# Optimization experiments

Measured on AMD Instinct MI355X. Metric: run time of the kernel, lower is better.

## Reference

```python
import jax, jax.numpy as jnp
import numpy as np

B = 64          # batch of trees
L = 10          # gated internal levels below the root
H = 256         # hidden_size
E = 256         # embed_size
V = 64          # embedding vocab (relation/role types)
TOTAL = 2 ** (L + 1) - 2   # heap layout: level i (1..L) has 2^i nodes at offset 2^i - 2


def setup_inputs() -> dict:
    key = jax.random.key(0)
    k = jax.random.split(key, 7)
    s = 0.05
    return {
        "node_ids": jax.random.randint(k[0], (B, TOTAL), 0, V, dtype=jnp.int32),
        "emb_table": jax.random.normal(k[1], (V, E), jnp.float32) * s,
        # W: x-projections, order (forget, input, output, update)
        "W": jax.random.normal(k[2], (4, E, H), jnp.float32) * s,
        "bW": jax.random.normal(k[3], (4, H), jnp.float32) * s,
        # U: hidden projections, [gate, child] with gate order
        # (forget_left, forget_right, input, output, update), child order (left, right)
        "U": jax.random.normal(k[4], (5, 2, H, H), jnp.float32) * s,
        "Ws": jax.random.normal(k[5], (2 * H, 3), jnp.float32) * s,
        "bs": jax.random.normal(k[6], (3,), jnp.float32) * s,
    }


def _tree_lstm(node_ids, emb_table, W, bW, U, Ws, bs):
    Bn, total = node_ids.shape
    Lv = int(np.log2(total + 2)) - 1          # number of gated levels (static)
    Hh = U.shape[-1]
    # Wforget is shared by both forget gates (as in the original module)
    gate_map = jnp.array([0, 0, 1, 2, 3])      # x-projection index per gate
    h = c = None
    for lev in range(Lv, 0, -1):               # leaves-up level order
        n = 2 ** lev
        off = 2 ** lev - 2
        ids = node_ids[:, off:off + n]         # [B, n]
        x = emb_table[ids]                     # [B, n, E]
        xg = jnp.einsum('bne,geh->gbnh', x, W) + bW[:, None, None, :]  # [4,B,n,H]
        if h is None:
            # deepest level: children are leaves -> zero h and c (init_hidden())
            hl = hr = cl = cr = jnp.zeros((Bn, n, Hh), x.dtype)
        else:
            hl, hr = h[:, 0::2], h[:, 1::2]
            cl, cr = c[:, 0::2], c[:, 1::2]
        pre = (jnp.einsum('bnh,ghk->gbnk', hl, U[:, 0])
               + jnp.einsum('bnh,ghk->gbnk', hr, U[:, 1])
               + xg[gate_map])                 # [5,B,n,H]
        f_l = jax.nn.sigmoid(pre[0])
        f_r = jax.nn.sigmoid(pre[1])
        i_g = jax.nn.sigmoid(pre[2])
        o_g = jax.nn.sigmoid(pre[3])
        u_g = jnp.tanh(pre[4])
        c = i_g * u_g + f_l * cl + f_r * cr
        h = o_g * jnp.tanh(c)
    # root: concatenate the two children's hidden states, then score
    root_hidden = jnp.concatenate([h[:, 0], h[:, 1]], axis=-1)   # [B, 2H]
    scores = root_hidden @ Ws + bs                               # [B, 3]
    return scores, root_hidden


def reference(node_ids, emb_table, W, bW, U, Ws, bs):
    return _tree_lstm(node_ids, emb_table, W, bW, U, Ws, bs)
```

## Files before the change

### kernel.cpp

```cpp
#include <hip/hip_runtime.h>
#include <hip/hip_bf16.h>
#include <stdint.h>
#include <math.h>


typedef __bf16 bf16x8 __attribute__((ext_vector_type(8)));
typedef float  f32x4  __attribute__((ext_vector_type(4)));
typedef int    i32x4  __attribute__((ext_vector_type(4)));

__device__ __forceinline__ float sigf(float x) { return 1.f / (1.f + __expf(-x)); }
__device__ __forceinline__ float tanhfast(float x) {
    return 1.f - 2.f / (__expf(2.f * x) + 1.f);
}

__global__ void xg_prep(const float* __restrict__ emb, const float* __restrict__ W,
                        const float* __restrict__ bW, float* __restrict__ xg4) {
    int g = blockIdx.x >> 6, v = blockIdx.x & 63, k = threadIdx.x;
    __shared__ float e[256];
    e[k] = emb[v * 256 + k];
    __syncthreads();
    float s = bW[g * 256 + k];
    const float* Wg = W + g * 65536 + k;
#pragma unroll 4
    for (int i = 0; i < 256; i++) s += e[i] * Wg[i * 256];
    xg4[(v * 256 + k) * 4 + g] = s;
}

__global__ void bt_prep(const float* __restrict__ U, __bf16* __restrict__ BtP) {
    int t = blockIdx.x * 256 + threadIdx.x;
    int g    = t >> 14;
    int r    = t & 16383;
    int ct   = r >> 10;
    int ks   = (r >> 6) & 15;
    int lane = t & 63;
    int lr = lane & 15, q = lane >> 4;
    int col = ct * 16 + lr;
    int kbase = ks * 32 + q * 8;
    bf16x8 v8;
#pragma unroll
    for (int e = 0; e < 8; e++) {
        int k = kbase + e;
        int s = k >> 8, kk = k & 255;
        v8[e] = (__bf16)U[((g * 2 + s) * 256 + kk) * 256 + col];
    }
    *(bf16x8*)(BtP + (long)t * 8) = v8;
}

__global__ void leaf_kernel(const int* __restrict__ ids, const float* __restrict__ xg4,
                            __bf16* __restrict__ h, __bf16* __restrict__ c) {
    int col = threadIdx.x;
    int r0 = blockIdx.x * 32;
    for (int r = r0; r < r0 + 32; r++) {
        int b = r >> 10, j = r & 1023;
        int id = ids[b * 2046 + 1022 + j];
        f32x4 xv = *(const f32x4*)(xg4 + (id * 256 + col) * 4);
        float ig = sigf(xv.y);
        float og = sigf(xv.z);
        float ug = tanhfast(xv.w);
        float cv = ig * ug;
        float hv = og * tanhfast(cv);
        h[r * 256 + col] = (__bf16)hv;
        c[r * 256 + col] = (__bf16)cv;
    }
}

__global__ __launch_bounds__(1024, 4) void level_kernel(
    const __bf16* __restrict__ A, const __bf16* __restrict__ Cprev,
    const __bf16* __restrict__ BtP, const float* __restrict__ xg4,
    const int* __restrict__ ids, __bf16* __restrict__ h_out,
    __bf16* __restrict__ c_out, float* __restrict__ rh_out, int lev, int M, int RG) {
    __shared__ __bf16 Blds[5 * 16 * 512];
    const int gid = blockIdx.x;
    int rg, ct;
    if ((RG & 7) == 0) {
        int xcd = gid & 7;
        int t   = gid >> 3;
        ct = t & 15;
        rg = ((t >> 4) << 3) | xcd;
    } else {
        rg = gid >> 4;
        ct = gid & 15;
    }
    const int tid  = threadIdx.x;
    const int wave = tid >> 6;
    const int lane = tid & 63;
    const int lr = lane & 15, q = lane >> 4;
    const long wrow = (long)rg * 512 + wave * 32;
    const bool active = (wrow < M);

#pragma unroll
    for (int i = 0; i < 5; i++) {
        int c = tid + i * 1024;
        int g = c >> 10;
        int r = c & 1023;
        i32x4 v = *(const i32x4*)(BtP + (long)(g * 16 + ct) * 8192 + r * 8);
        *(i32x4*)(&Blds[g * 8192 + r * 8]) = v;
    }

    const __bf16* Ap = A + (wrow + lr) * 512 + q * 8;
    bf16x8 af[4][2];
    if (active) {
#pragma unroll
        for (int mt = 0; mt < 2; mt++) {
            af[0][mt] = *(const bf16x8*)(Ap + mt * 8192);
            af[1][mt] = *(const bf16x8*)(Ap + mt * 8192 + 32);
            af[2][mt] = *(const bf16x8*)(Ap + mt * 8192 + 64);
        }
    }

    const int n = 1 << lev;
    const int gcol = ct * 16 + lr;
    int idv[2][4];
    __bf16 clv[2][4], crv[2][4];
    if (active) {
#pragma unroll
        for (int mt = 0; mt < 2; mt++)
#pragma unroll
            for (int v = 0; v < 4; v++) {
                long grow = wrow + mt * 16 + q * 4 + v;
                int b = (int)(grow >> lev);
                int j = (int)(grow & (n - 1));
                idv[mt][v] = ids[b * 2046 + (n - 2) + j];
                clv[mt][v] = Cprev[grow * 512 + gcol];
                crv[mt][v] = Cprev[grow * 512 + 256 + gcol];
            }
    }

    __syncthreads();

    if (active) {
        f32x4 acc[5][2];
#pragma unroll
        for (int g2 = 0; g2 < 5; g2++)
#pragma unroll
            for (int mt = 0; mt < 2; mt++) acc[g2][mt] = (f32x4){0.f, 0.f, 0.f, 0.f};

        bf16x8 bb[2][5];
#pragma unroll
        for (int g2 = 0; g2 < 5; g2++)
            bb[0][g2] = *(const bf16x8*)(&Blds[g2 * 8192 + lane * 8]);

#pragma unroll
        for (int s = 0; s < 16; s++) {
            if (s + 3 < 16) {
#pragma unroll
                for (int mt = 0; mt < 2; mt++)
                    af[(s + 3) & 3][mt] =
                        *(const bf16x8*)(Ap + mt * 8192 + (s + 3) * 32);
            }
            if (s + 1 < 16) {
#pragma unroll
                for (int g2 = 0; g2 < 5; g2++)
                    bb[(s + 1) & 1][g2] =
                        *(const bf16x8*)(&Blds[g2 * 8192 + (s + 1) * 512 + lane * 8]);
            }
#pragma unroll
            for (int g2 = 0; g2 < 5; g2++)
#pragma unroll
                for (int mt = 0; mt < 2; mt++)
                    acc[g2][mt] = __builtin_amdgcn_mfma_f32_16x16x32_bf16(
                        af[s & 3][mt], bb[s & 1][g2], acc[g2][mt], 0, 0, 0);
        }

#pragma unroll
        for (int mt = 0; mt < 2; mt++) {
#pragma unroll
            for (int v = 0; v < 4; v++) {
                long grow = wrow + mt * 16 + q * 4 + v;
                f32x4 xv = *(const f32x4*)(xg4 + (idv[mt][v] * 256 + gcol) * 4);
                float fl = sigf(acc[0][mt][v] + xv.x);
                float fr = sigf(acc[1][mt][v] + xv.x);
                float ig = sigf(acc[2][mt][v] + xv.y);
                float og = sigf(acc[3][mt][v] + xv.z);
                float ug = tanhfast(acc[4][mt][v] + xv.w);
                float cv = ig * ug + fl * (float)clv[mt][v] + fr * (float)crv[mt][v];
                float hv = og * tanhfast(cv);
                h_out[grow * 256 + gcol] = (__bf16)hv;
                c_out[grow * 256 + gcol] = (__bf16)cv;
                if (rh_out) rh_out[grow * 256 + gcol] = hv;
            }
        }
    }
}

__global__ void scores_kernel(const float* __restrict__ rh, const float* __restrict__ Ws,
                              const float* __restrict__ bs, float* __restrict__ out) {
    int b = blockIdx.x;
    int t = threadIdx.x >> 6, lane = threadIdx.x & 63;
    float s = 0.f;
    for (int i = lane; i < 512; i += 64) s += rh[b * 512 + i] * Ws[i * 3 + t];
    for (int o = 32; o > 0; o >>= 1) s += __shfl_down(s, o);
    if (lane == 0) out[b * 3 + t] = s + bs[t];
}

extern "C" void kernel_launch(void* const* d_in, const int* in_sizes, int n_in,
                              void* d_out, int out_size, void* d_ws, size_t ws_size,
                              hipStream_t stream) {
    const int*   ids = (const int*)  d_in[0];
    const float* emb = (const float*)d_in[1];
    const float* W   = (const float*)d_in[2];
    const float* bW  = (const float*)d_in[3];
    const float* U   = (const float*)d_in[4];
    const float* Ws  = (const float*)d_in[5];
    const float* bs  = (const float*)d_in[6];
    float* out = (float*)d_out;

    char* ws = (char*)d_ws;
    float*  xg4 = (float*)ws;
    __bf16* BtP = (__bf16*)(ws + 262144);
    __bf16* h0  = (__bf16*)(ws + 1572864);
    __bf16* c0  = (__bf16*)(ws + 35127296);
    __bf16* h1  = (__bf16*)(ws + 68681728);
    __bf16* c1  = (__bf16*)(ws + 85458944);

    xg_prep<<<dim3(256), dim3(256), 0, stream>>>(emb, W, bW, xg4);
    bt_prep<<<dim3(320), dim3(256), 0, stream>>>(U, BtP);
    leaf_kernel<<<dim3(2048), dim3(256), 0, stream>>>(ids, xg4, h0, c0);

    __bf16* hb[2] = {h0, h1};
    __bf16* cb[2] = {c0, c1};
    int cur = 0;
    for (int lev = 9; lev >= 1; lev--) {
        int M = 64 << lev;
        int RG = (M + 511) / 512;
        float* rh = (lev == 1) ? (out + 192) : nullptr;
        level_kernel<<<dim3(RG * 16), dim3(1024), 0, stream>>>(
            hb[cur], cb[cur], BtP, xg4, ids, hb[1 - cur], cb[1 - cur], rh, lev, M, RG);
        cur = 1 - cur;
    }
    scores_kernel<<<dim3(64), dim3(192), 0, stream>>>(out + 192, Ws, bs, out);
}
```

Baseline: 430.8 us.

## Fuse per-level launches into one persistent cooperative kernel with grid sync

Replaces nine separate level_kernel launches with a single cooperative persistent kernel of 256 blocks. Each block loads its column tile of U into LDS once, then loops over levels and row groups, separating levels with a threadfence plus grid.sync. This removes repeated launch and LDS reload costs, at the price of grid-wide barriers and fewer blocks on the large early levels. The A and B fragment prefetch is also changed to a three-stage ring.

```diff
diff --git a/kernel.cpp b/kernel.cpp
--- a/kernel.cpp
+++ b/kernel.cpp
@@ -1,8 +1,11 @@
 #include <hip/hip_runtime.h>
+#include <hip/hip_cooperative_groups.h>
 #include <hip/hip_bf16.h>
 #include <stdint.h>
 #include <math.h>
 
+
+namespace cg = cooperative_groups;
 
 typedef __bf16 bf16x8 __attribute__((ext_vector_type(8)));
 typedef float  f32x4  __attribute__((ext_vector_type(4)));
@@ -64,122 +67,127 @@
     }
 }
 
-__global__ __launch_bounds__(1024, 4) void level_kernel(
-    const __bf16* __restrict__ A, const __bf16* __restrict__ Cprev,
+__global__ __launch_bounds__(1024, 4) void tree_levels(
+    __bf16* __restrict__ h0, __bf16* __restrict__ c0,
+    __bf16* __restrict__ h1, __bf16* __restrict__ c1,
     const __bf16* __restrict__ BtP, const float* __restrict__ xg4,
-    const int* __restrict__ ids, __bf16* __restrict__ h_out,
-    __bf16* __restrict__ c_out, float* __restrict__ rh_out, int lev, int M, int RG) {
+    const int* __restrict__ ids, float* __restrict__ rh_base) {
     __shared__ __bf16 Blds[5 * 16 * 512];
-    const int gid = blockIdx.x;
-    int rg, ct;
-    if ((RG & 7) == 0) {
-        int xcd = gid & 7;
-        int t   = gid >> 3;
-        ct = t & 15;
-        rg = ((t >> 4) << 3) | xcd;
-    } else {
-        rg = gid >> 4;
-        ct = gid & 15;
-    }
+    cg::grid_group grid = cg::this_grid();
+
+    const int pid  = blockIdx.x;
+    const int xcd  = pid & 7;
+    const int ct   = (pid >> 3) & 15;
+    const int slot = pid >> 7;
     const int tid  = threadIdx.x;
     const int wave = tid >> 6;
     const int lane = tid & 63;
     const int lr = lane & 15, q = lane >> 4;
-    const long wrow = (long)rg * 512 + wave * 32;
-    const bool active = (wrow < M);
+    const int gcol = ct * 16 + lr;
 
 #pragma unroll
     for (int i = 0; i < 5; i++) {
-        int c = tid + i * 1024;
-        int g = c >> 10;
-        int r = c & 1023;
-        i32x4 v = *(const i32x4*)(BtP + (long)(g * 16 + ct) * 8192 + r * 8);
-        *(i32x4*)(&Blds[g * 8192 + r * 8]) = v;
-    }
-
-    const __bf16* Ap = A + (wrow + lr) * 512 + q * 8;
-    bf16x8 af[4][2];
-    if (active) {
-#pragma unroll
-        for (int mt = 0; mt < 2; mt++) {
-            af[0][mt] = *(const bf16x8*)(Ap + mt * 8192);
-            af[1][mt] = *(const bf16x8*)(Ap + mt * 8192 + 32);
-            af[2][mt] = *(const bf16x8*)(Ap + mt * 8192 + 64);
-        }
-    }
-
-    const int n = 1 << lev;
-    const int gcol = ct * 16 + lr;
-    int idv[2][4];
-    __bf16 clv[2][4], crv[2][4];
-    if (active) {
-#pragma unroll
-        for (int mt = 0; mt < 2; mt++)
-#pragma unroll
-            for (int v = 0; v < 4; v++) {
-                long grow = wrow + mt * 16 + q * 4 + v;
-                int b = (int)(grow >> lev);
-                int j = (int)(grow & (n - 1));
-                idv[mt][v] = ids[b * 2046 + (n - 2) + j];
-                clv[mt][v] = Cprev[grow * 512 + gcol];
-                crv[mt][v] = Cprev[grow * 512 + 256 + gcol];
-            }
-    }
-
+        int cc = tid + i * 1024;
+        int g = cc >> 10;
+        int r = cc & 1023;
+        *(i32x4*)(&Blds[g * 8192 + r * 8]) =
+            *(const i32x4*)(BtP + (long)(g * 16 + ct) * 8192 + r * 8);
+    }
     __syncthreads();
 
-    if (active) {
-        f32x4 acc[5][2];
-#pragma unroll
-        for (int g2 = 0; g2 < 5; g2++)
-#pragma unroll
-            for (int mt = 0; mt < 2; mt++) acc[g2][mt] = (f32x4){0.f, 0.f, 0.f, 0.f};
-
-        bf16x8 bb[2][5];
-#pragma unroll
-        for (int g2 = 0; g2 < 5; g2++)
-            bb[0][g2] = *(const bf16x8*)(&Blds[g2 * 8192 + lane * 8]);
-
-#pragma unroll
-        for (int s = 0; s < 16; s++) {
-            if (s + 3 < 16) {
+    for (int lev = 9; lev >= 1; lev--) {
+        const int M  = 64 << lev;
+        const int RG = (M + 511) >> 9;
+        const int p  = (9 - lev) & 1;
+        const __bf16* A  = p ? h1 : h0;
+        const __bf16* Cp = p ? c1 : c0;
+        __bf16* Ho = p ? h0 : h1;
+        __bf16* Co = p ? c0 : c1;
+        float* rh = (lev == 1) ? rh_base : nullptr;
+        const int n = 1 << lev;
+
+        for (int rg = xcd + 8 * slot; rg < RG; rg += 16) {
+            const long wrow = (long)rg * 512 + wave * 32;
+            if (wrow < M) {
+                const __bf16* Ap = A + (wrow + lr) * 512 + q * 8;
+                bf16x8 af[3][2];
+#pragma unroll
+                for (int mt = 0; mt < 2; mt++) {
+                    af[0][mt] = *(const bf16x8*)(Ap + mt * 8192);
+                    af[1][mt] = *(const bf16x8*)(Ap + mt * 8192 + 32);
+                }
+
+                int idv[2][4];
+                __bf16 clv[2][4], crv[2][4];
 #pragma unroll
                 for (int mt = 0; mt < 2; mt++)
-                    af[(s + 3) & 3][mt] =
-                        *(const bf16x8*)(Ap + mt * 8192 + (s + 3) * 32);
-            }
-            if (s + 1 < 16) {
+#pragma unroll
+                    for (int v = 0; v < 4; v++) {
+                        long grow = wrow + mt * 16 + q * 4 + v;
+                        int b = (int)(grow >> lev);
+                        int j = (int)(grow & (n - 1));
+                        idv[mt][v] = ids[b * 2046 + (n - 2) + j];
+                        clv[mt][v] = Cp[grow * 512 + gcol];
+                        crv[mt][v] = Cp[grow * 512 + 256 + gcol];
+                    }
+
+                f32x4 acc[5][2];
 #pragma unroll
                 for (int g2 = 0; g2 < 5; g2++)
-                    bb[(s + 1) & 1][g2] =
-                        *(const bf16x8*)(&Blds[g2 * 8192 + (s + 1) * 512 + lane * 8]);
-            }
-#pragma unroll
-            for (int g2 = 0; g2 < 5; g2++)
-#pragma unroll
-                for (int mt = 0; mt < 2; mt++)
-                    acc[g2][mt] = __builtin_amdgcn_mfma_f32_16x16x32_bf16(
-                        af[s & 3][mt], bb[s & 1][g2], acc[g2][mt], 0, 0, 0);
-        }
-
-#pragma unroll
-        for (int mt = 0; mt < 2; mt++) {
-#pragma unroll
-            for (int v = 0; v < 4; v++) {
-                long grow = wrow + mt * 16 + q * 4 + v;
-                f32x4 xv = *(const f32x4*)(xg4 + (idv[mt][v] * 256 + gcol) * 4);
-                float fl = sigf(acc[0][mt][v] + xv.x);
-                float fr = sigf(acc[1][mt][v] + xv.x);
-                float ig = sigf(acc[2][mt][v] + xv.y);
-                float og = sigf(acc[3][mt][v] + xv.z);
-                float ug = tanhfast(acc[4][mt][v] + xv.w);
-                float cv = ig * ug + fl * (float)clv[mt][v] + fr * (float)crv[mt][v];
-                float hv = og * tanhfast(cv);
-                h_out[grow * 256 + gcol] = (__bf16)hv;
-                c_out[grow * 256 + gcol] = (__bf16)cv;
-                if (rh_out) rh_out[grow * 256 + gcol] = hv;
+#pragma unroll
+                    for (int mt = 0; mt < 2; mt++)
+                        acc[g2][mt] = (f32x4){0.f, 0.f, 0.f, 0.f};
+
+                bf16x8 bb[3][5];
+#pragma unroll
+                for (int g2 = 0; g2 < 5; g2++) {
+                    bb[0][g2] = *(const bf16x8*)(&Blds[g2 * 8192 + lane * 8]);
+                    bb[1][g2] = *(const bf16x8*)(&Blds[g2 * 8192 + 512 + lane * 8]);
+                }
+
+#pragma unroll
+                for (int s = 0; s < 16; s++) {
+                    if (s + 2 < 16) {
+#pragma unroll
+                        for (int g2 = 0; g2 < 5; g2++)
+                            bb[(s + 2) % 3][g2] = *(const bf16x8*)(
+                                &Blds[g2 * 8192 + (s + 2) * 512 + lane * 8]);
+#pragma unroll
+                        for (int mt = 0; mt < 2; mt++)
+                            af[(s + 2) % 3][mt] =
+                                *(const bf16x8*)(Ap + mt * 8192 + (s + 2) * 32);
+                    }
+#pragma unroll
+                    for (int g2 = 0; g2 < 5; g2++)
+#pragma unroll
+                        for (int mt = 0; mt < 2; mt++)
+                            acc[g2][mt] = __builtin_amdgcn_mfma_f32_16x16x32_bf16(
+                                af[s % 3][mt], bb[s % 3][g2], acc[g2][mt], 0, 0, 0);
+                }
+
+#pragma unroll
+                for (int mt = 0; mt < 2; mt++) {
+#pragma unroll
+                    for (int v = 0; v < 4; v++) {
+                        long grow = wrow + mt * 16 + q * 4 + v;
+                        f32x4 xv = *(const f32x4*)(xg4 + (idv[mt][v] * 256 + gcol) * 4);
+                        float fl = sigf(acc[0][mt][v] + xv.x);
+                        float fr = sigf(acc[1][mt][v] + xv.x);
+                        float ig = sigf(acc[2][mt][v] + xv.y);
+                        float og = sigf(acc[3][mt][v] + xv.z);
+                        float ug = tanhfast(acc[4][mt][v] + xv.w);
+                        float cv = ig * ug + fl * (float)clv[mt][v]
+                                           + fr * (float)crv[mt][v];
+                        float hv = og * tanhfast(cv);
+                        Ho[grow * 256 + gcol] = (__bf16)hv;
+                        Co[grow * 256 + gcol] = (__bf16)cv;
+                        if (rh) rh[grow * 256 + gcol] = hv;
+                    }
+                }
             }
         }
+        __threadfence();
+        grid.sync();
     }
 }
 
@@ -217,16 +225,10 @@
     bt_prep<<<dim3(320), dim3(256), 0, stream>>>(U, BtP);
     leaf_kernel<<<dim3(2048), dim3(256), 0, stream>>>(ids, xg4, h0, c0);
 
-    __bf16* hb[2] = {h0, h1};
-    __bf16* cb[2] = {c0, c1};
-    int cur = 0;
-    for (int lev = 9; lev >= 1; lev--) {
-        int M = 64 << lev;
-        int RG = (M + 511) / 512;
-        float* rh = (lev == 1) ? (out + 192) : nullptr;
-        level_kernel<<<dim3(RG * 16), dim3(1024), 0, stream>>>(
-            hb[cur], cb[cur], BtP, xg4, ids, hb[1 - cur], cb[1 - cur], rh, lev, M, RG);
-        cur = 1 - cur;
-    }
+    float* rh_base = out + 192;
+    void* args[] = {(void*)&h0, (void*)&c0, (void*)&h1, (void*)&c1,
+                    (void*)&BtP, (void*)&xg4, (void*)&ids, (void*)&rh_base};
+    hipLaunchCooperativeKernel(tree_levels, dim3(256), dim3(1024), args, 0, stream);
+
     scores_kernel<<<dim3(64), dim3(192), 0, stream>>>(out + 192, Ws, bs, out);
 }
```

Measured after the change: 1.413 ms. +228.1%, slower.

## Make level kernel persistent over row groups to reuse the LDS weight tile

Applied to the files above, without the earlier changes.

The grid is capped at 16 row-group slots per column tile, and each block loops over several row groups, loading its 5-gate B tile into LDS once and reusing it. A-fragment prefetch depth drops from three to two stages and carries across row-group boundaries so the next group's loads overlap the current MFMAs. This cuts repeated global-to-LDS B loads on the large levels but reduces the number of blocks, which at level 9 (RG=64) means 256 blocks instead of 1024 and may lower occupancy and latency hiding. The XCD-aware block remapping is dropped in favour of a simple slot/column split.

```diff
diff --git a/kernel.cpp b/kernel.cpp
--- a/kernel.cpp
+++ b/kernel.cpp
@@ -68,118 +68,124 @@
     const __bf16* __restrict__ A, const __bf16* __restrict__ Cprev,
     const __bf16* __restrict__ BtP, const float* __restrict__ xg4,
     const int* __restrict__ ids, __bf16* __restrict__ h_out,
-    __bf16* __restrict__ c_out, float* __restrict__ rh_out, int lev, int M, int RG) {
+    __bf16* __restrict__ c_out, float* __restrict__ rh_out,
+    int lev, int M, int RG, int NB, int NB16) {
     __shared__ __bf16 Blds[5 * 16 * 512];
     const int gid = blockIdx.x;
-    int rg, ct;
-    if ((RG & 7) == 0) {
-        int xcd = gid & 7;
-        int t   = gid >> 3;
-        ct = t & 15;
-        rg = ((t >> 4) << 3) | xcd;
-    } else {
-        rg = gid >> 4;
-        ct = gid & 15;
-    }
+    int rgslot, ct;
+    if (NB16) { rgslot = gid & 15; ct = gid >> 4; }
+    else      { rgslot = gid % NB; ct = gid / NB; }
     const int tid  = threadIdx.x;
     const int wave = tid >> 6;
     const int lane = tid & 63;
     const int lr = lane & 15, q = lane >> 4;
-    const long wrow = (long)rg * 512 + wave * 32;
-    const bool active = (wrow < M);
+    const int gcol = ct * 16 + lr;
+    const int n = 1 << lev;
 
 #pragma unroll
     for (int i = 0; i < 5; i++) {
-        int c = tid + i * 1024;
-        int g = c >> 10;
-        int r = c & 1023;
-        i32x4 v = *(const i32x4*)(BtP + (long)(g * 16 + ct) * 8192 + r * 8);
-        *(i32x4*)(&Blds[g * 8192 + r * 8]) = v;
-    }
-
+        int cc = tid + i * 1024;
+        int g = cc >> 10;
+        int r = cc & 1023;
+        *(i32x4*)(&Blds[g * 8192 + r * 8]) =
+            *(const i32x4*)(BtP + (long)(g * 16 + ct) * 8192 + r * 8);
+    }
+    __syncthreads();
+
+    int rg0 = rgslot;
+    long wrow = (long)rg0 * 512 + wave * 32;
     const __bf16* Ap = A + (wrow + lr) * 512 + q * 8;
     bf16x8 af[4][2];
-    if (active) {
+    if (wrow < M) {
 #pragma unroll
         for (int mt = 0; mt < 2; mt++) {
             af[0][mt] = *(const bf16x8*)(Ap + mt * 8192);
             af[1][mt] = *(const bf16x8*)(Ap + mt * 8192 + 32);
-            af[2][mt] = *(const bf16x8*)(Ap + mt * 8192 + 64);
         }
     }
 
-    const int n = 1 << lev;
-    const int gcol = ct * 16 + lr;
-    int idv[2][4];
-    __bf16 clv[2][4], crv[2][4];
-    if (active) {
-#pragma unroll
-        for (int mt = 0; mt < 2; mt++)
-#pragma unroll
-            for (int v = 0; v < 4; v++) {
-                long grow = wrow + mt * 16 + q * 4 + v;
-                int b = (int)(grow >> lev);
-                int j = (int)(grow & (n - 1));
-                idv[mt][v] = ids[b * 2046 + (n - 2) + j];
-                clv[mt][v] = Cprev[grow * 512 + gcol];
-                crv[mt][v] = Cprev[grow * 512 + 256 + gcol];
+    for (int rg = rg0; rg < RG; rg += NB) {
+        wrow = (long)rg * 512 + wave * 32;
+        const bool active = (wrow < M);
+
+        int rgn = rg + NB;
+        long wrown = (rgn < RG) ? ((long)rgn * 512 + wave * 32) : wrow;
+        const __bf16* Apn = A + (wrown + lr) * 512 + q * 8;
+
+        int idv[2][4];
+        __bf16 clv[2][4], crv[2][4];
+        if (active) {
+#pragma unroll
+            for (int mt = 0; mt < 2; mt++)
+#pragma unroll
+                for (int v = 0; v < 4; v++) {
+                    long grow = wrow + mt * 16 + q * 4 + v;
+                    int b = (int)(grow >> lev);
+                    int j = (int)(grow & (n - 1));
+                    idv[mt][v] = ids[b * 2046 + (n - 2) + j];
+                    clv[mt][v] = Cprev[grow * 512 + gcol];
+                    crv[mt][v] = Cprev[grow * 512 + 256 + gcol];
+                }
+        }
+
+        if (active) {
+            f32x4 acc[5][2];
+#pragma unroll
+            for (int g2 = 0; g2 < 5; g2++)
+#pragma unroll
+                for (int mt = 0; mt < 2; mt++)
+                    acc[g2][mt] = (f32x4){0.f, 0.f, 0.f, 0.f};
+
+            bf16x8 bb[2][5];
+#pragma unroll
+            for (int g2 = 0; g2 < 5; g2++)
+                bb[0][g2] = *(const bf16x8*)(&Blds[g2 * 8192 + lane * 8]);
+
+#pragma unroll
+            for (int s = 0; s < 16; s++) {
+                {
+                    int sp = s + 2;
+                    const __bf16* P = (sp < 16) ? Ap : Apn;
+                    int so = sp & 15;
+#pragma unroll
+                    for (int mt = 0; mt < 2; mt++)
+                        af[sp & 3][mt] = *(const bf16x8*)(P + mt * 8192 + so * 32);
+                }
+                if (s + 1 < 16) {
+#pragma unroll
+                    for (int g2 = 0; g2 < 5; g2++)
+                        bb[(s + 1) & 1][g2] =
+                            *(const bf16x8*)(&Blds[g2 * 8192 + (s + 1) * 512 + lane * 8]);
+                }
+#pragma unroll
+                for (int g2 = 0; g2 < 5; g2++)
+#pragma unroll
+                    for (int mt = 0; mt < 2; mt++)
+                        acc[g2][mt] = __builtin_amdgcn_mfma_f32_16x16x32_bf16(
+                            af[s & 3][mt], bb[s & 1][g2], acc[g2][mt], 0, 0, 0);
             }
-    }
-
-    __syncthreads();
-
-    if (active) {
-        f32x4 acc[5][2];
-#pragma unroll
-        for (int g2 = 0; g2 < 5; g2++)
-#pragma unroll
-            for (int mt = 0; mt < 2; mt++) acc[g2][mt] = (f32x4){0.f, 0.f, 0.f, 0.f};
-
-        bf16x8 bb[2][5];
-#pragma unroll
-        for (int g2 = 0; g2 < 5; g2++)
-            bb[0][g2] = *(const bf16x8*)(&Blds[g2 * 8192 + lane * 8]);
-
-#pragma unroll
-        for (int s = 0; s < 16; s++) {
-            if (s + 3 < 16) {
-#pragma unroll
-                for (int mt = 0; mt < 2; mt++)
-                    af[(s + 3) & 3][mt] =
-                        *(const bf16x8*)(Ap + mt * 8192 + (s + 3) * 32);
-            }
-            if (s + 1 < 16) {
-#pragma unroll
-                for (int g2 = 0; g2 < 5; g2++)
-                    bb[(s + 1) & 1][g2] =
-                        *(const bf16x8*)(&Blds[g2 * 8192 + (s + 1) * 512 + lane * 8]);
-            }
-#pragma unroll
-            for (int g2 = 0; g2 < 5; g2++)
-#pragma unroll
-                for (int mt = 0; mt < 2; mt++)
-                    acc[g2][mt] = __builtin_amdgcn_mfma_f32_16x16x32_bf16(
-                        af[s & 3][mt], bb[s & 1][g2], acc[g2][mt], 0, 0, 0);
-        }
-
-#pragma unroll
-        for (int mt = 0; mt < 2; mt++) {
-#pragma unroll
-            for (int v = 0; v < 4; v++) {
-                long grow = wrow + mt * 16 + q * 4 + v;
-                f32x4 xv = *(const f32x4*)(xg4 + (idv[mt][v] * 256 + gcol) * 4);
-                float fl = sigf(acc[0][mt][v] + xv.x);
-                float fr = sigf(acc[1][mt][v] + xv.x);
-                float ig = sigf(acc[2][mt][v] + xv.y);
-                float og = sigf(acc[3][mt][v] + xv.z);
-                float ug = tanhfast(acc[4][mt][v] + xv.w);
-                float cv = ig * ug + fl * (float)clv[mt][v] + fr * (float)crv[mt][v];
-                float hv = og * tanhfast(cv);
-                h_out[grow * 256 + gcol] = (__bf16)hv;
-                c_out[grow * 256 + gcol] = (__bf16)cv;
-                if (rh_out) rh_out[grow * 256 + gcol] = hv;
+
+#pragma unroll
+            for (int mt = 0; mt < 2; mt++) {
+#pragma unroll
+                for (int v = 0; v < 4; v++) {
+                    long grow = wrow + mt * 16 + q * 4 + v;
+                    f32x4 xv = *(const f32x4*)(xg4 + (idv[mt][v] * 256 + gcol) * 4);
+                    float fl = sigf(acc[0][mt][v] + xv.x);
+                    float fr = sigf(acc[1][mt][v] + xv.x);
+                    float ig = sigf(acc[2][mt][v] + xv.y);
+                    float og = sigf(acc[3][mt][v] + xv.z);
+                    float ug = tanhfast(acc[4][mt][v] + xv.w);
+                    float cv = ig * ug + fl * (float)clv[mt][v]
+                                       + fr * (float)crv[mt][v];
+                    float hv = og * tanhfast(cv);
+                    h_out[grow * 256 + gcol] = (__bf16)hv;
+                    c_out[grow * 256 + gcol] = (__bf16)cv;
+                    if (rh_out) rh_out[grow * 256 + gcol] = hv;
+                }
             }
         }
+        Ap = Apn;
     }
 }
 
@@ -222,10 +228,12 @@
     int cur = 0;
     for (int lev = 9; lev >= 1; lev--) {
         int M = 64 << lev;
-        int RG = (M + 511) / 512;
+        int RG = M >> 9; if (RG < 1) RG = 1;
+        int NB = (RG < 16) ? RG : 16;
         float* rh = (lev == 1) ? (out + 192) : nullptr;
-        level_kernel<<<dim3(RG * 16), dim3(1024), 0, stream>>>(
-            hb[cur], cb[cur], BtP, xg4, ids, hb[1 - cur], cb[1 - cur], rh, lev, M, RG);
+        level_kernel<<<dim3(16 * NB), dim3(1024), 0, stream>>>(
+            hb[cur], cb[cur], BtP, xg4, ids, hb[1 - cur], cb[1 - cur], rh,
+            lev, M, RG, NB, (NB == 16) ? 1 : 0);
         cur = 1 - cur;
     }
     scores_kernel<<<dim3(64), dim3(192), 0, stream>>>(out + 192, Ws, bs, out);
```

New measurement: 415.7 us. 1.04x faster.
